# Optimization experiments

Measured on AMD Instinct MI355X. Metric: run time of the kernel, lower is better.

## Reference

```python
import jax, jax.numpy as jnp
import numpy as np

B, CIN, COUT, L = 16, 128, 128, 4096  # kernel_size == L required by the broadcast in the source
STRIDE, DIL, PAD = 1, 1, 0


def setup_inputs() -> dict:
    key = jax.random.key(0)
    kx, kw, kb = jax.random.split(key, 3)
    x = jax.random.normal(kx, (B, CIN, L), dtype=jnp.float32)
    # source does weight.data.int() then .float() in forward -> integer-truncated randn
    weight = jnp.trunc(jax.random.normal(kw, (COUT, CIN, L), dtype=jnp.float32))
    bias = jax.random.normal(kb, (COUT,), dtype=jnp.float32)
    return {"x": x, "weight": weight, "bias": bias}


def reference(x, weight, bias):
    # padding=0 -> F.pad is a no-op; output_size = (L + 2*0 - 1*(K-1) - 1)//1 + 1 = 1
    out_size = (L + 2 * PAD - DIL * (L - 1) - 1) // STRIDE + 1  # == 1
    x_f = jnp.fft.fft(x, axis=2)            # [B, Cin, L] complex64
    w_f = jnp.fft.fft(weight, axis=2)       # [Cout, Cin, L] complex64
    # faithful math of (x_f[:,None] * w_f[None]).sum(dim=2), expressed as a
    # per-frequency complex contraction to avoid the O(B*Cout*Cin*L) intermediate
    out_f = jnp.einsum('bil,oil->bol', x_f, w_f)  # [B, Cout, L]
    out = jnp.fft.ifft(out_f, axis=2).real
    out = out + bias[None, :, None]
    return out[:, :, :out_size]
```

## Files before the change

### kernel.cpp

```cpp
#include <hip/hip_runtime.h>


constexpr int LEN   = 4096;
constexpr int CIN_  = 128;
constexpr int COUT_ = 128;
constexpr int BATCH = 16;

__global__ void init_out_kernel(const float* __restrict__ bias, float* __restrict__ out) {
    int t = blockIdx.x * 256 + threadIdx.x;
    if (t < BATCH * COUT_) out[t] = bias[t & (COUT_ - 1)];
}

__device__ __forceinline__ void gload_lds4(const float* g, float* l) {
    __builtin_amdgcn_global_load_lds(
        (const __attribute__((address_space(1))) unsigned int*)g,
        (__attribute__((address_space(3))) unsigned int*)l, 4, 0, 0);
}

__device__ __forceinline__ void stage_chunk(const float* __restrict__ x, float* dst_base,
                                            int ci, int m0, int wv, int lane) {
#pragma unroll
    for (int bb = 0; bb < 2; ++bb) {
        const int b = 2 * wv + bb;
        const float* xc = x + ((b * CIN_ + ci) << 12);
        float* dstb = dst_base + (b << 9);
#pragma unroll
        for (int t = 0; t < 8; ++t) {
            const int n = (LEN - m0 - (t << 6) - lane) & (LEN - 1);
            gload_lds4(xc + n, dstb + (t << 6));
        }
    }
}

__global__ __launch_bounds__(512, 1)
void conv_fft_dot_kernel(const float* __restrict__ x, const float* __restrict__ w,
                         float* __restrict__ out) {
    __shared__ float lds[17408];

    const int tid   = threadIdx.x;
    const int lane  = tid & 63;
    const int wv    = __builtin_amdgcn_readfirstlane(tid >> 6);
    const int bk    = blockIdx.x;
    const int ot    = bk >> 7;
    const int ci    = bk & 127;
    const int obase = ot * 32 + wv * 4;

    float acc[16][4];
#pragma unroll
    for (int b = 0; b < 16; ++b)
#pragma unroll
        for (int j = 0; j < 4; ++j) acc[b][j] = 0.f;

    stage_chunk(x, lds, ci, 0, wv, lane);
    __syncthreads();

#pragma unroll 1
    for (int q = 0; q < 8; ++q) {
        const int m0 = q << 9;
        const float4* __restrict__ xb = (const float4*)(lds + ((q & 1) << 13));

        float4 wA[4], wB[4];
#pragma unroll
        for (int j = 0; j < 4; ++j) {
            const float4* wp = (const float4*)(w + (((obase + j) * CIN_ + ci) << 12) + m0);
            wA[j] = wp[lane];
            wB[j] = wp[64 + lane];
        }

        if (q < 7)
            stage_chunk(x, lds + (((q + 1) & 1) << 13), ci, (q + 1) << 9, wv, lane);

#pragma unroll
        for (int b = 0; b < 16; ++b) {
            const float4 xv = xb[(b << 7) + lane];
#pragma unroll
            for (int j = 0; j < 4; ++j) {
                acc[b][j] += xv.x * wA[j].x;
                acc[b][j] += xv.y * wA[j].y;
                acc[b][j] += xv.z * wA[j].z;
                acc[b][j] += xv.w * wA[j].w;
            }
        }
#pragma unroll
        for (int b = 0; b < 16; ++b) {
            const float4 xv = xb[(b << 7) + 64 + lane];
#pragma unroll
            for (int j = 0; j < 4; ++j) {
                acc[b][j] += xv.x * wB[j].x;
                acc[b][j] += xv.y * wB[j].y;
                acc[b][j] += xv.z * wB[j].z;
                acc[b][j] += xv.w * wB[j].w;
            }
        }
        __syncthreads();
    }

#pragma unroll
    for (int pass = 0; pass < 2; ++pass) {
        if (pass) __syncthreads();
#pragma unroll
        for (int b = 0; b < 16; ++b) {
            lds[(wv * 32 + b * 2 + 0) * 68 + lane] = acc[b][pass * 2 + 0];
            lds[(wv * 32 + b * 2 + 1) * 68 + lane] = acc[b][pass * 2 + 1];
        }
        __syncthreads();
        if (tid < 256) {
            const float4* row = (const float4*)(lds + tid * 68);
            float sum = 0.f;
#pragma unroll
            for (int l = 0; l < 16; ++l) {
                const float4 v = row[l];
                sum += v.x + v.y + v.z + v.w;
            }
            const int wv2 = tid >> 5, r = tid & 31;
            const int b = r >> 1, jj = r & 1;
            const int o = ot * 32 + wv2 * 4 + pass * 2 + jj;
            atomicAdd(out + b * COUT_ + o, sum);
        }
    }
}

extern "C" void kernel_launch(void* const* d_in, const int* in_sizes, int n_in,
                              void* d_out, int out_size, void* d_ws, size_t ws_size,
                              hipStream_t stream) {
    const float* x    = (const float*)d_in[0];
    const float* wgt  = (const float*)d_in[1];
    const float* bias = (const float*)d_in[2];
    float* out = (float*)d_out;
    (void)in_sizes; (void)n_in; (void)d_ws; (void)ws_size; (void)out_size;

    init_out_kernel<<<8, 256, 0, stream>>>(bias, out);
    conv_fft_dot_kernel<<<512, 512, 0, stream>>>(x, wgt, out);
}
```

Before: 403.9 us.

## Halve outputs per block, double grid, and software-pipeline weight loads with manual waitcnt

Each block now covers 16 output channels instead of 32, so the grid doubles to 1024 blocks and launch bounds allow two blocks per CU through lower register pressure. Weight loads are split into half-chunks and prefetched one stage ahead. The full __syncthreads is replaced with a manual s_waitcnt vmcnt(2) plus s_barrier, so the x staging and weight prefetch can overlap the FMA work. The cost is that each x chunk is staged twice as often across blocks, and the hand-counted vmcnt is fragile if the compiler reorders loads.

```diff
diff --git a/kernel.cpp b/kernel.cpp
--- a/kernel.cpp
+++ b/kernel.cpp
@@ -32,7 +32,7 @@
     }
 }
 
-__global__ __launch_bounds__(512, 1)
+__global__ __launch_bounds__(512, 2)
 void conv_fft_dot_kernel(const float* __restrict__ x, const float* __restrict__ w,
                          float* __restrict__ out) {
     __shared__ float lds[17408];
@@ -43,29 +43,30 @@
     const int bk    = blockIdx.x;
     const int ot    = bk >> 7;
     const int ci    = bk & 127;
-    const int obase = ot * 32 + wv * 4;
+    const int obase = ot * 16 + wv * 2;
 
-    float acc[16][4];
+    const float* wr0 = w + (((obase + 0) * CIN_ + ci) << 12);
+    const float* wr1 = w + (((obase + 1) * CIN_ + ci) << 12);
+
+    float acc[16][2];
 #pragma unroll
-    for (int b = 0; b < 16; ++b)
-#pragma unroll
-        for (int j = 0; j < 4; ++j) acc[b][j] = 0.f;
+    for (int b = 0; b < 16; ++b) { acc[b][0] = 0.f; acc[b][1] = 0.f; }
 
     stage_chunk(x, lds, ci, 0, wv, lane);
-    __syncthreads();
+    __builtin_amdgcn_sched_barrier(0);
+    float4 wa0 = ((const float4*)wr0)[lane];
+    float4 wa1 = ((const float4*)wr1)[lane];
+    asm volatile("s_waitcnt vmcnt(2)" ::: "memory");
+    __builtin_amdgcn_s_barrier();
+    __builtin_amdgcn_sched_barrier(0);
 
 #pragma unroll 1
     for (int q = 0; q < 8; ++q) {
         const int m0 = q << 9;
         const float4* __restrict__ xb = (const float4*)(lds + ((q & 1) << 13));
 
-        float4 wA[4], wB[4];
-#pragma unroll
-        for (int j = 0; j < 4; ++j) {
-            const float4* wp = (const float4*)(w + (((obase + j) * CIN_ + ci) << 12) + m0);
-            wA[j] = wp[lane];
-            wB[j] = wp[64 + lane];
-        }
+        float4 wb0 = ((const float4*)(wr0 + m0 + 256))[lane];
+        float4 wb1 = ((const float4*)(wr1 + m0 + 256))[lane];
 
         if (q < 7)
             stage_chunk(x, lds + (((q + 1) & 1) << 13), ci, (q + 1) << 9, wv, lane);
@@ -73,50 +74,54 @@
 #pragma unroll
         for (int b = 0; b < 16; ++b) {
             const float4 xv = xb[(b << 7) + lane];
-#pragma unroll
-            for (int j = 0; j < 4; ++j) {
-                acc[b][j] += xv.x * wA[j].x;
-                acc[b][j] += xv.y * wA[j].y;
-                acc[b][j] += xv.z * wA[j].z;
-                acc[b][j] += xv.w * wA[j].w;
-            }
+            acc[b][0] += xv.x * wa0.x; acc[b][0] += xv.y * wa0.y;
+            acc[b][0] += xv.z * wa0.z; acc[b][0] += xv.w * wa0.w;
+            acc[b][1] += xv.x * wa1.x; acc[b][1] += xv.y * wa1.y;
+            acc[b][1] += xv.z * wa1.z; acc[b][1] += xv.w * wa1.w;
         }
+
+        __builtin_amdgcn_sched_barrier(0);
+
+        if (q < 7) {
+            wa0 = ((const float4*)(wr0 + m0 + 512))[lane];
+            wa1 = ((const float4*)(wr1 + m0 + 512))[lane];
+        }
+
 #pragma unroll
         for (int b = 0; b < 16; ++b) {
             const float4 xv = xb[(b << 7) + 64 + lane];
-#pragma unroll
-            for (int j = 0; j < 4; ++j) {
-                acc[b][j] += xv.x * wB[j].x;
-                acc[b][j] += xv.y * wB[j].y;
-                acc[b][j] += xv.z * wB[j].z;
-                acc[b][j] += xv.w * wB[j].w;
-            }
+            acc[b][0] += xv.x * wb0.x; acc[b][0] += xv.y * wb0.y;
+            acc[b][0] += xv.z * wb0.z; acc[b][0] += xv.w * wb0.w;
+            acc[b][1] += xv.x * wb1.x; acc[b][1] += xv.y * wb1.y;
+            acc[b][1] += xv.z * wb1.z; acc[b][1] += xv.w * wb1.w;
         }
-        __syncthreads();
+
+        if (q < 7) {
+            asm volatile("s_waitcnt vmcnt(2)" ::: "memory");
+            __builtin_amdgcn_s_barrier();
+            __builtin_amdgcn_sched_barrier(0);
+        }
     }
 
+    __syncthreads();
 #pragma unroll
-    for (int pass = 0; pass < 2; ++pass) {
-        if (pass) __syncthreads();
+    for (int b = 0; b < 16; ++b) {
+        lds[(wv * 32 + b * 2 + 0) * 68 + lane] = acc[b][0];
+        lds[(wv * 32 + b * 2 + 1) * 68 + lane] = acc[b][1];
+    }
+    __syncthreads();
+    if (tid < 256) {
+        const float4* row = (const float4*)(lds + tid * 68);
+        float sum = 0.f;
 #pragma unroll
-        for (int b = 0; b < 16; ++b) {
-            lds[(wv * 32 + b * 2 + 0) * 68 + lane] = acc[b][pass * 2 + 0];
-            lds[(wv * 32 + b * 2 + 1) * 68 + lane] = acc[b][pass * 2 + 1];
+        for (int l = 0; l < 16; ++l) {
+            const float4 v = row[l];
+            sum += v.x + v.y + v.z + v.w;
         }
-        __syncthreads();
-        if (tid < 256) {
-            const float4* row = (const float4*)(lds + tid * 68);
-            float sum = 0.f;
-#pragma unroll
-            for (int l = 0; l < 16; ++l) {
-                const float4 v = row[l];
-                sum += v.x + v.y + v.z + v.w;
-            }
-            const int wv2 = tid >> 5, r = tid & 31;
-            const int b = r >> 1, jj = r & 1;
-            const int o = ot * 32 + wv2 * 4 + pass * 2 + jj;
-            atomicAdd(out + b * COUT_ + o, sum);
-        }
+        const int wv2 = tid >> 5, r = tid & 31;
+        const int b = r >> 1, jj = r & 1;
+        const int o = ot * 16 + wv2 * 2 + jj;
+        atomicAdd(out + b * COUT_ + o, sum);
     }
 }
 
@@ -130,5 +135,5 @@
     (void)in_sizes; (void)n_in; (void)d_ws; (void)ws_size; (void)out_size;
 
     init_out_kernel<<<8, 256, 0, stream>>>(bias, out);
-    conv_fft_dot_kernel<<<512, 512, 0, stream>>>(x, wgt, out);
+    conv_fft_dot_kernel<<<1024, 512, 0, stream>>>(x, wgt, out);
 }
```

After: 393.6 us. 1.03x faster.

## Software-pipeline weight loads with nontemporal loads and explicit vmcnt barriers

Applied to the files above, without the earlier changes.

Weight float4 loads are now nontemporal and split into two halves that are prefetched one phase ahead: the next chunk's first half is issued during the second-half compute. The per-iteration __syncthreads is replaced by a partial s_waitcnt vmcnt(4) plus s_barrier, so the in-flight weight loads need not drain before the barrier. Launch bounds now request 2 blocks per CU. The goal is to hide HBM weight-streaming latency behind FMA work. The risks are tighter register limits from the occupancy hint, and reliance on precise vmcnt ordering between LDS-direct loads and register loads.

```diff
diff --git a/kernel.cpp b/kernel.cpp
--- a/kernel.cpp
+++ b/kernel.cpp
@@ -6,9 +6,15 @@
 constexpr int COUT_ = 128;
 constexpr int BATCH = 16;
 
+typedef float f32x4 __attribute__((ext_vector_type(4)));
+
 __global__ void init_out_kernel(const float* __restrict__ bias, float* __restrict__ out) {
     int t = blockIdx.x * 256 + threadIdx.x;
     if (t < BATCH * COUT_) out[t] = bias[t & (COUT_ - 1)];
+}
+
+__device__ __forceinline__ f32x4 ntload4(const float* p) {
+    return __builtin_nontemporal_load((const f32x4*)p);
 }
 
 __device__ __forceinline__ void gload_lds4(const float* g, float* l) {
@@ -32,7 +38,7 @@
     }
 }
 
-__global__ __launch_bounds__(512, 1)
+__global__ __launch_bounds__(512, 2)
 void conv_fft_dot_kernel(const float* __restrict__ x, const float* __restrict__ w,
                          float* __restrict__ out) {
     __shared__ float lds[17408];
@@ -45,6 +51,12 @@
     const int ci    = bk & 127;
     const int obase = ot * 32 + wv * 4;
 
+    const float* wr0 = w + (((obase + 0) * CIN_ + ci) << 12);
+    const float* wr1 = w + (((obase + 1) * CIN_ + ci) << 12);
+    const float* wr2 = w + (((obase + 2) * CIN_ + ci) << 12);
+    const float* wr3 = w + (((obase + 3) * CIN_ + ci) << 12);
+    const int lo16 = lane << 2;
+
     float acc[16][4];
 #pragma unroll
     for (int b = 0; b < 16; ++b)
@@ -52,20 +64,24 @@
         for (int j = 0; j < 4; ++j) acc[b][j] = 0.f;
 
     stage_chunk(x, lds, ci, 0, wv, lane);
-    __syncthreads();
+    __builtin_amdgcn_sched_barrier(0);
+    f32x4 wa[4];
+    wa[0] = ntload4(wr0 + lo16); wa[1] = ntload4(wr1 + lo16);
+    wa[2] = ntload4(wr2 + lo16); wa[3] = ntload4(wr3 + lo16);
+    asm volatile("s_waitcnt vmcnt(4)" ::: "memory");
+    __builtin_amdgcn_s_barrier();
+    __builtin_amdgcn_sched_barrier(0);
 
 #pragma unroll 1
     for (int q = 0; q < 8; ++q) {
         const int m0 = q << 9;
         const float4* __restrict__ xb = (const float4*)(lds + ((q & 1) << 13));
 
-        float4 wA[4], wB[4];
-#pragma unroll
-        for (int j = 0; j < 4; ++j) {
-            const float4* wp = (const float4*)(w + (((obase + j) * CIN_ + ci) << 12) + m0);
-            wA[j] = wp[lane];
-            wB[j] = wp[64 + lane];
-        }
+        f32x4 wb[4];
+        wb[0] = ntload4(wr0 + m0 + 256 + lo16);
+        wb[1] = ntload4(wr1 + m0 + 256 + lo16);
+        wb[2] = ntload4(wr2 + m0 + 256 + lo16);
+        wb[3] = ntload4(wr3 + m0 + 256 + lo16);
 
         if (q < 7)
             stage_chunk(x, lds + (((q + 1) & 1) << 13), ci, (q + 1) << 9, wv, lane);
@@ -75,26 +91,42 @@
             const float4 xv = xb[(b << 7) + lane];
 #pragma unroll
             for (int j = 0; j < 4; ++j) {
-                acc[b][j] += xv.x * wA[j].x;
-                acc[b][j] += xv.y * wA[j].y;
-                acc[b][j] += xv.z * wA[j].z;
-                acc[b][j] += xv.w * wA[j].w;
+                acc[b][j] += xv.x * wa[j].x;
+                acc[b][j] += xv.y * wa[j].y;
+                acc[b][j] += xv.z * wa[j].z;
+                acc[b][j] += xv.w * wa[j].w;
             }
         }
+
+        __builtin_amdgcn_sched_barrier(0);
+
+        if (q < 7) {
+            wa[0] = ntload4(wr0 + m0 + 512 + lo16);
+            wa[1] = ntload4(wr1 + m0 + 512 + lo16);
+            wa[2] = ntload4(wr2 + m0 + 512 + lo16);
+            wa[3] = ntload4(wr3 + m0 + 512 + lo16);
+        }
+
 #pragma unroll
         for (int b = 0; b < 16; ++b) {
             const float4 xv = xb[(b << 7) + 64 + lane];
 #pragma unroll
             for (int j = 0; j < 4; ++j) {
-                acc[b][j] += xv.x * wB[j].x;
-                acc[b][j] += xv.y * wB[j].y;
-                acc[b][j] += xv.z * wB[j].z;
-                acc[b][j] += xv.w * wB[j].w;
+                acc[b][j] += xv.x * wb[j].x;
+                acc[b][j] += xv.y * wb[j].y;
+                acc[b][j] += xv.z * wb[j].z;
+                acc[b][j] += xv.w * wb[j].w;
             }
         }
-        __syncthreads();
+
+        if (q < 7) {
+            asm volatile("s_waitcnt vmcnt(4)" ::: "memory");
+            __builtin_amdgcn_s_barrier();
+            __builtin_amdgcn_sched_barrier(0);
+        }
     }
 
+    __syncthreads();
 #pragma unroll
     for (int pass = 0; pass < 2; ++pass) {
         if (pass) __syncthreads();
```

New measurement: 382.3 us. 1.06x faster.

## Split work by input channel and tap chunk, cache x in LDS, stream weights

Applied to the files above, without the earlier changes.

The dot kernel is reorganised so each block owns one input channel and one 512-tap chunk and loads that x chunk into LDS once. It then loops over all output channels in groups of 16, streaming weights with nontemporal loads and prefetching the next group's weights during compute. Each output group is reduced per wave through a small LDS scratch and flushed with atomics. This removes the per-iteration x double-buffer staging and block-wide barriers and allows two 256-thread blocks per CU. In exchange it issues many more atomic adds and does more LDS reductions.

```diff
diff --git a/kernel.cpp b/kernel.cpp
--- a/kernel.cpp
+++ b/kernel.cpp
@@ -6,9 +6,15 @@
 constexpr int COUT_ = 128;
 constexpr int BATCH = 16;
 
+typedef float f32x4 __attribute__((ext_vector_type(4)));
+
 __global__ void init_out_kernel(const float* __restrict__ bias, float* __restrict__ out) {
     int t = blockIdx.x * 256 + threadIdx.x;
     if (t < BATCH * COUT_) out[t] = bias[t & (COUT_ - 1)];
+}
+
+__device__ __forceinline__ f32x4 ntload4(const float* p) {
+    return __builtin_nontemporal_load((const f32x4*)p);
 }
 
 __device__ __forceinline__ void gload_lds4(const float* g, float* l) {
@@ -17,33 +23,39 @@
         (__attribute__((address_space(3))) unsigned int*)l, 4, 0, 0);
 }
 
-__device__ __forceinline__ void stage_chunk(const float* __restrict__ x, float* dst_base,
-                                            int ci, int m0, int wv, int lane) {
+__global__ __launch_bounds__(256, 2)
+void conv_fft_dot_kernel(const float* __restrict__ x, const float* __restrict__ w,
+                         float* __restrict__ out) {
+    __shared__ float xls[8192];
+    __shared__ float fl[4 * 16 * 66];
+
+    const int tid  = threadIdx.x;
+    const int lane = tid & 63;
+    const int wv   = __builtin_amdgcn_readfirstlane(tid >> 6);
+    const int bk   = blockIdx.x;
+    const int ms   = bk >> 7;
+    const int ci   = bk & 127;
+    const int m0   = ms << 9;
+
 #pragma unroll
-    for (int bb = 0; bb < 2; ++bb) {
-        const int b = 2 * wv + bb;
+    for (int bb = 0; bb < 4; ++bb) {
+        const int b = 4 * wv + bb;
         const float* xc = x + ((b * CIN_ + ci) << 12);
-        float* dstb = dst_base + (b << 9);
+        float* dst = xls + (b << 9);
 #pragma unroll
         for (int t = 0; t < 8; ++t) {
             const int n = (LEN - m0 - (t << 6) - lane) & (LEN - 1);
-            gload_lds4(xc + n, dstb + (t << 6));
+            gload_lds4(xc + n, dst + (t << 6));
         }
     }
-}
-
-__global__ __launch_bounds__(512, 1)
-void conv_fft_dot_kernel(const float* __restrict__ x, const float* __restrict__ w,
-                         float* __restrict__ out) {
-    __shared__ float lds[17408];
-
-    const int tid   = threadIdx.x;
-    const int lane  = tid & 63;
-    const int wv    = __builtin_amdgcn_readfirstlane(tid >> 6);
-    const int bk    = blockIdx.x;
-    const int ot    = bk >> 7;
-    const int ci    = bk & 127;
-    const int obase = ot * 32 + wv * 4;
+    f32x4 wc[8];
+#pragma unroll
+    for (int j = 0; j < 4; ++j) {
+        const float* wr = w + ((((wv * 4 + j) << 7) + ci) << 12) + m0;
+        wc[j]     = ntload4(wr + (lane << 2));
+        wc[4 + j] = ntload4(wr + 256 + (lane << 2));
+    }
+    __syncthreads();
 
     float acc[16][4];
 #pragma unroll
@@ -51,71 +63,53 @@
 #pragma unroll
         for (int j = 0; j < 4; ++j) acc[b][j] = 0.f;
 
-    stage_chunk(x, lds, ci, 0, wv, lane);
-    __syncthreads();
+    const float4* xls4 = (const float4*)xls;
+    float* fr = fl + wv * (16 * 66);
 
 #pragma unroll 1
-    for (int q = 0; q < 8; ++q) {
-        const int m0 = q << 9;
-        const float4* __restrict__ xb = (const float4*)(lds + ((q & 1) << 13));
-
-        float4 wA[4], wB[4];
-#pragma unroll
-        for (int j = 0; j < 4; ++j) {
-            const float4* wp = (const float4*)(w + (((obase + j) * CIN_ + ci) << 12) + m0);
-            wA[j] = wp[lane];
-            wB[j] = wp[64 + lane];
-        }
-
-        if (q < 7)
-            stage_chunk(x, lds + (((q + 1) & 1) << 13), ci, (q + 1) << 9, wv, lane);
-
+    for (int u = 0; u < 8; ++u) {
 #pragma unroll
         for (int b = 0; b < 16; ++b) {
-            const float4 xv = xb[(b << 7) + lane];
+            const float4 xv0 = xls4[(b << 7) + lane];
+            const float4 xv1 = xls4[(b << 7) + 64 + lane];
 #pragma unroll
             for (int j = 0; j < 4; ++j) {
-                acc[b][j] += xv.x * wA[j].x;
-                acc[b][j] += xv.y * wA[j].y;
-                acc[b][j] += xv.z * wA[j].z;
-                acc[b][j] += xv.w * wA[j].w;
+                acc[b][j] += xv0.x * wc[j].x + xv0.y * wc[j].y
+                           + xv0.z * wc[j].z + xv0.w * wc[j].w;
+                acc[b][j] += xv1.x * wc[4 + j].x + xv1.y * wc[4 + j].y
+                           + xv1.z * wc[4 + j].z + xv1.w * wc[4 + j].w;
             }
         }
-#pragma unroll
-        for (int b = 0; b < 16; ++b) {
-            const float4 xv = xb[(b << 7) + 64 + lane];
+        if (u < 7) {
+            const int row = (u + 1) * 16 + wv * 4;
 #pragma unroll
             for (int j = 0; j < 4; ++j) {
-                acc[b][j] += xv.x * wB[j].x;
-                acc[b][j] += xv.y * wB[j].y;
-                acc[b][j] += xv.z * wB[j].z;
-                acc[b][j] += xv.w * wB[j].w;
+                const float* wr = w + ((((row + j) << 7) + ci) << 12) + m0;
+                wc[j]     = ntload4(wr + (lane << 2));
+                wc[4 + j] = ntload4(wr + 256 + (lane << 2));
             }
         }
-        __syncthreads();
-    }
-
+        __builtin_amdgcn_sched_barrier(0);
 #pragma unroll
-    for (int pass = 0; pass < 2; ++pass) {
-        if (pass) __syncthreads();
+        for (int p = 0; p < 4; ++p) {
 #pragma unroll
-        for (int b = 0; b < 16; ++b) {
-            lds[(wv * 32 + b * 2 + 0) * 68 + lane] = acc[b][pass * 2 + 0];
-            lds[(wv * 32 + b * 2 + 1) * 68 + lane] = acc[b][pass * 2 + 1];
-        }
-        __syncthreads();
-        if (tid < 256) {
-            const float4* row = (const float4*)(lds + tid * 68);
-            float sum = 0.f;
+            for (int bb = 0; bb < 4; ++bb)
 #pragma unroll
-            for (int l = 0; l < 16; ++l) {
-                const float4 v = row[l];
-                sum += v.x + v.y + v.z + v.w;
-            }
-            const int wv2 = tid >> 5, r = tid & 31;
-            const int b = r >> 1, jj = r & 1;
-            const int o = ot * 32 + wv2 * 4 + pass * 2 + jj;
-            atomicAdd(out + b * COUT_ + o, sum);
+                for (int j = 0; j < 4; ++j)
+                    fr[(bb * 4 + j) * 66 + lane] = acc[p * 4 + bb][j];
+            const int r = lane & 15, c = lane >> 4;
+            const float* rowp = fr + r * 66 + c * 16;
+            float s = 0.f;
+#pragma unroll
+            for (int k = 0; k < 8; ++k) s += rowp[2 * k] + rowp[2 * k + 1];
+            const int b = p * 4 + (r >> 2);
+            const int o = u * 16 + wv * 4 + (r & 3);
+            atomicAdd(out + b * COUT_ + o, s);
+#pragma unroll
+            for (int bb = 0; bb < 4; ++bb)
+#pragma unroll
+                for (int j = 0; j < 4; ++j)
+                    acc[p * 4 + bb][j] = 0.f;
         }
     }
 }
@@ -130,5 +124,5 @@
     (void)in_sizes; (void)n_in; (void)d_ws; (void)ws_size; (void)out_size;
 
     init_out_kernel<<<8, 256, 0, stream>>>(bias, out);
-    conv_fft_dot_kernel<<<512, 512, 0, stream>>>(x, wgt, out);
+    conv_fft_dot_kernel<<<1024, 256, 0, stream>>>(x, wgt, out);
 }
```

After: 833.0 us. 2.06x slower.
